# Kernel tuning notes

Measured on AMD Instinct MI355X. Metric: run time of the kernel, lower is better.

The kernel has to match this reference:

```python
import jax, jax.numpy as jnp
import numpy as np

B, N, D, C, Q = 8, 2048, 512, 4096, 4


def l2norm(x):
    return x / jnp.maximum(jnp.linalg.norm(x, axis=-1, keepdims=True), 1e-12)


def rotate_to(src, tgt):
    # rotation-trick transform: rotate src onto tgt, rotation detached
    sg = jax.lax.stop_gradient
    ns = jnp.linalg.norm(src, axis=-1, keepdims=True)
    nt = jnp.linalg.norm(tgt, axis=-1, keepdims=True)
    u = src / ns
    q = tgt / nt
    w = sg(l2norm(u + q))  # Householder bisector, detached
    e = src
    r = (e
         - 2.0 * jnp.sum(e * w, axis=-1, keepdims=True) * w
         + 2.0 * jnp.sum(e * sg(u), axis=-1, keepdims=True) * q)
    return r * sg(nt / ns)


def setup_inputs() -> dict:
    key = jax.random.key(0)
    k1, k2, k3 = jax.random.split(key, 3)
    x = jax.random.normal(k1, (B, N, D), jnp.float32)
    codebooks = jax.random.normal(k2, (Q, C, D), jnp.float32) * D ** -0.5
    weights = jax.random.normal(k3, (Q, D, D), jnp.float32) * D ** -0.5
    return {"x": x, "codebooks": codebooks, "weights": weights}


def reference(x, codebooks, weights):
    sg = jax.lax.stop_gradient
    num_q = codebooks.shape[0]
    residual = x
    quantized_out = jnp.zeros_like(x)
    all_idx, all_loss = [], []
    for i in range(num_q):
        implicit_cb = codebooks[i] @ weights[i].T  # Linear(dim,dim,bias=False)
        cb_n = l2norm(implicit_cb)                 # [C, D]
        x_n = l2norm(residual)                     # [B, N, D]
        # argmax of cosine similarity (no_grad in torch)
        sim = jnp.einsum('bnd,cd->bnc', sg(x_n), sg(cb_n))
        idx = jnp.argmax(sim, axis=-1)             # [B, N]
        quant = cb_n[idx]                          # [B, N, D]
        commit = (jnp.mean((sg(x_n) - quant) ** 2)
                  + 0.25 * jnp.mean((x_n - sg(quant)) ** 2))
        quant = rotate_to(x_n, quant)
        residual = residual - sg(quant)
        quantized_out = quantized_out + quant
        all_idx.append(idx)
        all_loss.append(commit)
    return quantized_out, jnp.stack(all_idx, axis=-1), jnp.stack(all_loss, axis=-1)
```

## Files before the change

kernel.cpp:

```cpp
#include <hip/hip_runtime.h>
#include <math.h>

#define RR 16384
#define DD 512
#define CC 4096
#define QQ 4
#define NB 32
#define NG 64
#define QOUT_SZ (RR*DD)
#define IDX_OFF QOUT_SZ
#define LOSS_OFF (QOUT_SZ + RR*QQ)
#define LOSS_COEF (1.25f / 8388608.0f)
#define NBLK_FIN (RR/4)

#define WS_RESID 0
#define WS_CBN   (RR*DD)
#define WS_RNRM  (WS_CBN + CC*DD)
#define WS_PV    (WS_RNRM + RR)
#define WS_PI    (WS_PV + RR*32*4)
#define WS_F16   (WS_PI + RR*32*4 + 4)
#define F16_A 0
#define F16_B (RR*DD)

typedef _Float16 f16x8 __attribute__((ext_vector_type(8)));
typedef float f32x4 __attribute__((ext_vector_type(4)));

__device__ __forceinline__ float waveSum(float v) {
#pragma unroll
    for (int m = 1; m < 64; m <<= 1) v += __shfl_xor(v, m, 64);
    return v;
}

template <int N>
__device__ __forceinline__ void waveSumN(float* v) {
#pragma unroll
    for (int m = 1; m < 64; m <<= 1) {
#pragma unroll
        for (int j = 0; j < N; ++j) v[j] += __shfl_xor(v[j], m, 64);
    }
}

__device__ __forceinline__ unsigned packKey(float v, int c) {
    unsigned u = __float_as_uint(v);
    u ^= (unsigned)((int)u >> 31) | 0x80000000u;
    return (u & 0xFFFFF000u) | (unsigned)(4095 - c);
}

__device__ __forceinline__ void ceDesc(unsigned &a, unsigned &b) {
    unsigned mn = a > b ? b : a;
    a = a > b ? a : b;
    b = mn;
}

__device__ __forceinline__ void merge4(unsigned k[4],
                                       unsigned b0, unsigned b1,
                                       unsigned b2, unsigned b3) {
    k[0] = k[0] > b3 ? k[0] : b3;
    k[1] = k[1] > b2 ? k[1] : b2;
    k[2] = k[2] > b1 ? k[2] : b1;
    k[3] = k[3] > b0 ? k[3] : b0;
    ceDesc(k[0], k[2]); ceDesc(k[1], k[3]);
    ceDesc(k[0], k[1]); ceDesc(k[2], k[3]);
}

__device__ __forceinline__ void merge4Shfl(unsigned k[4], int m) {
    unsigned b0 = __shfl_xor(k[0], m, 64);
    unsigned b1 = __shfl_xor(k[1], m, 64);
    unsigned b2 = __shfl_xor(k[2], m, 64);
    unsigned b3 = __shfl_xor(k[3], m, 64);
    merge4(k, b0, b1, b2, b3);
}

__global__ void initK(const float* __restrict__ x, float* __restrict__ resid,
                      float* __restrict__ dout) {
    int i = blockIdx.x * blockDim.x + threadIdx.x;
    int stride = gridDim.x * blockDim.x;
    for (; i < QOUT_SZ; i += stride) { resid[i] = x[i]; dout[i] = 0.0f; }
}

__global__ __launch_bounds__(256) void gemmCbK(const float* __restrict__ A,
                                               const float* __restrict__ W,
                                               float* __restrict__ out) {
    __shared__ float As[32][64];
    __shared__ float Bs[32][64];
    int t = threadIdx.x;
    int tx = t & 15, ty = t >> 4;
    int cBase = blockIdx.x * 64;
    int dBase = blockIdx.y * 64;
    int f = t & 7;
    int mq = t >> 3;
    float acc[4][4] = {};
    for (int k0 = 0; k0 < DD; k0 += 32) {
        __syncthreads();
#pragma unroll
        for (int p = 0; p < 2; ++p) {
            int m = mq + p * 32;
            float4 av = *(const float4*)&A[(size_t)(cBase + m) * DD + k0 + f * 4];
            As[f*4+0][m] = av.x; As[f*4+1][m] = av.y; As[f*4+2][m] = av.z; As[f*4+3][m] = av.w;
            float4 wv = *(const float4*)&W[(size_t)(dBase + m) * DD + k0 + f * 4];
            Bs[f*4+0][m] = wv.x; Bs[f*4+1][m] = wv.y; Bs[f*4+2][m] = wv.z; Bs[f*4+3][m] = wv.w;
        }
        __syncthreads();
#pragma unroll
        for (int kk = 0; kk < 32; ++kk) {
            float4 a4 = *(const float4*)&As[kk][ty * 4];
            float4 b4 = *(const float4*)&Bs[kk][tx * 4];
            float a[4] = {a4.x, a4.y, a4.z, a4.w};
            float b[4] = {b4.x, b4.y, b4.z, b4.w};
#pragma unroll
            for (int i = 0; i < 4; ++i)
#pragma unroll
                for (int j = 0; j < 4; ++j) acc[i][j] += a[i] * b[j];
        }
    }
#pragma unroll
    for (int i = 0; i < 4; ++i) {
        float4 v = make_float4(acc[i][0], acc[i][1], acc[i][2], acc[i][3]);
        *(float4*)&out[(size_t)(cBase + ty * 4 + i) * DD + dBase + tx * 4] = v;
    }
}

__global__ void rowNormCvtK(float* __restrict__ buf, _Float16* __restrict__ bf16) {
    int wave = threadIdx.x >> 6, lane = threadIdx.x & 63;
    int row = blockIdx.x * 4 + wave;
    float* p = buf + (size_t)row * DD;
    float4 v0 = *(float4*)&p[lane * 8];
    float4 v1 = *(float4*)&p[lane * 8 + 4];
    float ss = v0.x*v0.x + v0.y*v0.y + v0.z*v0.z + v0.w*v0.w
             + v1.x*v1.x + v1.y*v1.y + v1.z*v1.z + v1.w*v1.w;
    ss = waveSum(ss);
    float nrm = fmaxf(sqrtf(ss), 1e-12f);
    float vals[8] = {v0.x/nrm, v0.y/nrm, v0.z/nrm, v0.w/nrm,
                     v1.x/nrm, v1.y/nrm, v1.z/nrm, v1.w/nrm};
    *(float4*)&p[lane * 8]     = make_float4(vals[0], vals[1], vals[2], vals[3]);
    *(float4*)&p[lane * 8 + 4] = make_float4(vals[4], vals[5], vals[6], vals[7]);
    f16x8 hv;
#pragma unroll
    for (int j = 0; j < 8; ++j) hv[j] = (_Float16)vals[j];
    *(f16x8*)&bf16[(size_t)row * DD + lane * 8] = hv;
}

__global__ void residCvtK(const float* __restrict__ resid,
                          float* __restrict__ rnrm, _Float16* __restrict__ af16) {
    int wave = threadIdx.x >> 6, lane = threadIdx.x & 63;
    int row = blockIdx.x * 4 + wave;
    const float* p = resid + (size_t)row * DD;
    float4 v0 = *(const float4*)&p[lane * 8];
    float4 v1 = *(const float4*)&p[lane * 8 + 4];
    float vals[8] = {v0.x, v0.y, v0.z, v0.w, v1.x, v1.y, v1.z, v1.w};
    float ss = 0.f;
#pragma unroll
    for (int j = 0; j < 8; ++j) ss += vals[j] * vals[j];
    ss = waveSum(ss);
    if (lane == 0) rnrm[row] = fmaxf(sqrtf(ss), 1e-12f);
    f16x8 hv;
#pragma unroll
    for (int j = 0; j < 8; ++j) hv[j] = (_Float16)vals[j];
    *(f16x8*)&af16[(size_t)row * DD + lane * 8] = hv;
}

__global__ __launch_bounds__(512)
void simMfmaK(
    const _Float16* __restrict__ Af16, const _Float16* __restrict__ Bf16,
    unsigned* __restrict__ pk) {
    __shared__ _Float16 Alds[128 * 64];
    __shared__ _Float16 Blds[128 * 64];
    int t = threadIdx.x, w = t >> 6, lane = t & 63;
    int rowBase = blockIdx.x * 128;
    int cBase = blockIdx.y * 128;
    int mbase = (w & 3) * 32, nbase = (w >> 2) * 64;
    int l15 = lane & 15, quad = lane >> 4;

    f32x4 acc[2][4];
#pragma unroll
    for (int i = 0; i < 2; ++i)
#pragma unroll
        for (int j = 0; j < 4; ++j) acc[i][j] = (f32x4){0.f, 0.f, 0.f, 0.f};

    int rsub = lane >> 3;
    int swz = (lane & 7) ^ rsub;

    for (int k0 = 0; k0 < DD; k0 += 64) {
        __syncthreads();
#pragma unroll
        for (int j = 0; j < 2; ++j) {
            int rA = rowBase + j * 64 + 8 * w + rsub;
            int rB = cBase + j * 64 + 8 * w + rsub;
            __builtin_amdgcn_global_load_lds(
                (const __attribute__((address_space(1))) void*)&Af16[(size_t)rA * DD + k0 + swz * 8],
                (__attribute__((address_space(3))) void*)&Alds[(j * 64 + 8 * w) * 64], 16, 0, 0);
            __builtin_amdgcn_global_load_lds(
                (const __attribute__((address_space(1))) void*)&Bf16[(size_t)rB * DD + k0 + swz * 8],
                (__attribute__((address_space(3))) void*)&Blds[(j * 64 + 8 * w) * 64], 16, 0, 0);
        }
        __syncthreads();
#pragma unroll
        for (int kh = 0; kh < 2; ++kh) {
            int chunk = (kh * 4 + quad) ^ (l15 & 7);
            f16x8 af[2];
#pragma unroll
            for (int tm = 0; tm < 2; ++tm)
                af[tm] = *(const f16x8*)&Alds[(mbase + tm * 16 + l15) * 64 + chunk * 8];
#pragma unroll
            for (int tn = 0; tn < 4; ++tn) {
                f16x8 bf = *(const f16x8*)&Blds[(nbase + tn * 16 + l15) * 64 + chunk * 8];
#pragma unroll
                for (int tm = 0; tm < 2; ++tm)
                    acc[tm][tn] = __builtin_amdgcn_mfma_f32_16x16x32_f16(
                        af[tm], bf, acc[tm][tn], 0, 0, 0);
            }
        }
    }

    int gkey = (cBase >> 6) + (w >> 2);
#pragma unroll
    for (int tm = 0; tm < 2; ++tm) {
#pragma unroll
        for (int r = 0; r < 4; ++r) {
            unsigned t0 = packKey(acc[tm][0][r], cBase + nbase + 0 * 16 + l15);
            unsigned t1 = packKey(acc[tm][1][r], cBase + nbase + 1 * 16 + l15);
            unsigned t2 = packKey(acc[tm][2][r], cBase + nbase + 2 * 16 + l15);
            unsigned t3 = packKey(acc[tm][3][r], cBase + nbase + 3 * 16 + l15);
            ceDesc(t0, t1); ceDesc(t2, t3);
            unsigned k0 = t0 > t2 ? t0 : t2;
            unsigned mn = t0 > t2 ? t2 : t0;
            unsigned mx = t1 > t3 ? t1 : t3;
            unsigned k1 = mn > mx ? mn : mx;
#pragma unroll
            for (int m = 1; m < 16; m <<= 1) {
                unsigned b0 = __shfl_xor(k0, m, 64);
                unsigned b1 = __shfl_xor(k1, m, 64);
                unsigned m0 = k0 > b0 ? k0 : b0;
                unsigned n0 = k0 > b0 ? b0 : k0;
                unsigned m1 = k1 > b1 ? k1 : b1;
                k0 = m0;
                k1 = n0 > m1 ? n0 : m1;
            }
            if (l15 == 0) {
                int rowg = rowBase + mbase + tm * 16 + quad * 4 + r;
                *(uint2*)&pk[(size_t)rowg * 128 + gkey * 2] = make_uint2(k0, k1);
            }
        }
    }
}

__global__ void finalizeK(float* __restrict__ resid,
                          float* __restrict__ rnrm,
                          const float* __restrict__ cbn,
                          const unsigned* __restrict__ pk,
                          float* __restrict__ dout,
                          float* __restrict__ lossPart,
                          _Float16* __restrict__ af16, int q) {
    __shared__ float sL[4];
    int wave = threadIdx.x >> 6, lane = threadIdx.x & 63;
    int row = blockIdx.x * 4 + wave;
    float* xr = resid + (size_t)row * DD;
    float nrm = rnrm[row];
    float4 a0 = *(float4*)&xr[lane * 8];
    float4 a1 = *(float4*)&xr[lane * 8 + 4];
    float orig[8] = {a0.x,a0.y,a0.z,a0.w,a1.x,a1.y,a1.z,a1.w};
    float x[8];
#pragma unroll
    for (int j = 0; j < 8; ++j) x[j] = orig[j] / nrm;

    uint2 kp = *(const uint2*)&pk[(size_t)row * 128 + lane * 2];
    unsigned k[4] = {kp.x, kp.y, 0u, 0u};
#pragma unroll
    for (int m = 1; m < 64; m <<= 1) merge4Shfl(k, m);
    int cand[4];
#pragma unroll
    for (int j = 0; j < 4; ++j)
        cand[j] = 4095 - (int)(__shfl(k[j], 0, 64) & 0xFFFu);

    float cv[4][8];
#pragma unroll
    for (int j = 0; j < 4; ++j) {
        const float* cbj = cbn + (size_t)cand[j] * DD;
        float4 c0 = *(const float4*)&cbj[lane * 8];
        float4 c1 = *(const float4*)&cbj[lane * 8 + 4];
        cv[j][0]=c0.x; cv[j][1]=c0.y; cv[j][2]=c0.z; cv[j][3]=c0.w;
        cv[j][4]=c1.x; cv[j][5]=c1.y; cv[j][6]=c1.z; cv[j][7]=c1.w;
    }
    float s[4];
#pragma unroll
    for (int j = 0; j < 4; ++j) {
        float acc = 0.f;
#pragma unroll
        for (int e = 0; e < 8; ++e) acc += x[e] * cv[j][e];
        s[j] = acc;
    }
    waveSumN<4>(s);
    float sBest = -3e38f; int idx = 0x7fffffff, sel = 0;
#pragma unroll
    for (int j = 0; j < 4; ++j) {
        if (s[j] > sBest || (s[j] == sBest && cand[j] < idx)) {
            sBest = s[j]; idx = cand[j]; sel = j;
        }
    }

    float qv[8];
#pragma unroll
    for (int e = 0; e < 8; ++e)
        qv[e] = sel == 0 ? cv[0][e] : sel == 1 ? cv[1][e]
              : sel == 2 ? cv[2][e] : cv[3][e];

    float red3[3] = {0.f, 0.f, 0.f};
#pragma unroll
    for (int j = 0; j < 8; ++j) {
        red3[0] += x[j] * x[j];
        red3[1] += qv[j] * qv[j];
        float d = x[j] - qv[j];
        red3[2] += d * d;
    }
    waveSumN<3>(red3);
    float ns = sqrtf(red3[0]), nt = sqrtf(red3[1]), lrow = red3[2];

    float u[8], qn[8], wv[8];
    float nw2 = 0.f;
#pragma unroll
    for (int j = 0; j < 8; ++j) {
        u[j] = x[j] / ns;
        qn[j] = qv[j] / nt;
        wv[j] = u[j] + qn[j];
        nw2 += wv[j] * wv[j];
    }
    nw2 = waveSum(nw2);
    float nw = fmaxf(sqrtf(nw2), 1e-12f);
    float red2[2] = {0.f, 0.f};
#pragma unroll
    for (int j = 0; j < 8; ++j) {
        wv[j] = wv[j] / nw;
        red2[0] += x[j] * wv[j];
        red2[1] += x[j] * u[j];
    }
    waveSumN<2>(red2);
    float dew = red2[0], deu = red2[1];
    float scale = nt / ns;

    float r[8], nres[8];
    float ss = 0.f;
#pragma unroll
    for (int j = 0; j < 8; ++j) {
        r[j] = (x[j] - 2.0f * dew * wv[j] + 2.0f * deu * qn[j]) * scale;
        nres[j] = orig[j] - r[j];
        ss += nres[j] * nres[j];
    }

    *(float4*)&xr[lane * 8]     = make_float4(nres[0], nres[1], nres[2], nres[3]);
    *(float4*)&xr[lane * 8 + 4] = make_float4(nres[4], nres[5], nres[6], nres[7]);
    ss = waveSum(ss);
    if (lane == 0) rnrm[row] = fmaxf(sqrtf(ss), 1e-12f);
    f16x8 hv;
#pragma unroll
    for (int j = 0; j < 8; ++j) hv[j] = (_Float16)nres[j];
    *(f16x8*)&af16[(size_t)row * DD + lane * 8] = hv;

    float* op = dout + (size_t)row * DD;
    float4 o0 = *(float4*)&op[lane * 8];
    float4 o1 = *(float4*)&op[lane * 8 + 4];
    o0.x += r[0]; o0.y += r[1]; o0.z += r[2]; o0.w += r[3];
    o1.x += r[4]; o1.y += r[5]; o1.z += r[6]; o1.w += r[7];
    *(float4*)&op[lane * 8] = o0;
    *(float4*)&op[lane * 8 + 4] = o1;

    if (lane == 0) {
        dout[IDX_OFF + row * 4 + q] = (float)idx;
        sL[wave] = lrow;
    }
    __syncthreads();
    if (threadIdx.x == 0) {
        lossPart[(size_t)q * NBLK_FIN + blockIdx.x] =
            (sL[0] + sL[1] + sL[2] + sL[3]) * LOSS_COEF;
    }
}

__global__ void lossWriteK(const float* __restrict__ lossPart,
                           float* __restrict__ dout) {
    int q = threadIdx.x >> 6, lane = threadIdx.x & 63;
    float s = 0.f;
    for (int i = lane; i < NBLK_FIN; i += 64)
        s += lossPart[(size_t)q * NBLK_FIN + i];
    s = waveSum(s);
    if (lane == 0) dout[LOSS_OFF + q] = s;
}

extern "C" void kernel_launch(void* const* d_in, const int* in_sizes, int n_in,
                              void* d_out, int out_size, void* d_ws, size_t ws_size,
                              hipStream_t stream) {
    const float* x = (const float*)d_in[0];
    const float* codebooks = (const float*)d_in[1];
    const float* weights = (const float*)d_in[2];
    float* dout = (float*)d_out;
    float* w = (float*)d_ws;

    float* resid = w + WS_RESID;
    float* cbn   = w + WS_CBN;
    float* rnrm  = w + WS_RNRM;
    unsigned* pk = (unsigned*)(w + WS_PV);
    float* lossPart = w + WS_PI;
    _Float16* f16base = (_Float16*)(w + WS_F16);
    _Float16* Af16 = f16base + F16_A;
    _Float16* Bf16 = f16base + F16_B;

    initK<<<4096, 256, 0, stream>>>(x, resid, dout);
    residCvtK<<<RR / 4, 256, 0, stream>>>(resid, rnrm, Af16);

    for (int q = 0; q < QQ; ++q) {
        gemmCbK<<<dim3(CC / 64, DD / 64), 256, 0, stream>>>(
            codebooks + (size_t)q * CC * DD, weights + (size_t)q * DD * DD, cbn);
        rowNormCvtK<<<CC / 4, 256, 0, stream>>>(cbn, Bf16);
        simMfmaK<<<dim3(RR / 128, CC / 128), 512, 0, stream>>>(Af16, Bf16, pk);
        finalizeK<<<RR / 4, 256, 0, stream>>>(resid, rnrm, cbn, pk,
                                              dout, lossPart, Af16, q);
    }
    lossWriteK<<<1, 256, 0, stream>>>(lossPart, dout);
}
```

Before: 891.7 us.

## Replace LDS-staged similarity GEMM with direct global-to-register MFMA loads

The similarity kernel no longer stages A and B tiles through shared memory with barriers. Each wave now loads its MFMA fragments straight from global memory into registers, double-buffered across k-steps. The block tile shrinks to 128x64 with 256 threads, and the launch grid is adjusted to match. This removes LDS traffic and __syncthreads, but it loses the cross-wave reuse that LDS gave: every wave rereads the same B rows from global memory or L2, which raises cache and memory load.

New measurement: 1.844 ms. 2.07x slower.

```diff
diff --git a/kernel.cpp b/kernel.cpp
--- a/kernel.cpp
+++ b/kernel.cpp
@@ -5,7 +5,6 @@
 #define DD 512
 #define CC 4096
 #define QQ 4
-#define NB 32
 #define NG 64
 #define QOUT_SZ (RR*DD)
 #define IDX_OFF QOUT_SZ
@@ -159,16 +158,14 @@
     *(f16x8*)&af16[(size_t)row * DD + lane * 8] = hv;
 }
 
-__global__ __launch_bounds__(512)
+__global__ __launch_bounds__(256)
 void simMfmaK(
     const _Float16* __restrict__ Af16, const _Float16* __restrict__ Bf16,
     unsigned* __restrict__ pk) {
-    __shared__ _Float16 Alds[128 * 64];
-    __shared__ _Float16 Blds[128 * 64];
     int t = threadIdx.x, w = t >> 6, lane = t & 63;
     int rowBase = blockIdx.x * 128;
-    int cBase = blockIdx.y * 128;
-    int mbase = (w & 3) * 32, nbase = (w >> 2) * 64;
+    int cBase = blockIdx.y * 64;
+    int mbase = w * 32;
     int l15 = lane & 15, quad = lane >> 4;
 
     f32x4 acc[2][4];
@@ -177,50 +174,58 @@
 #pragma unroll
         for (int j = 0; j < 4; ++j) acc[i][j] = (f32x4){0.f, 0.f, 0.f, 0.f};
 
-    int rsub = lane >> 3;
-    int swz = (lane & 7) ^ rsub;
-
-    for (int k0 = 0; k0 < DD; k0 += 64) {
-        __syncthreads();
-#pragma unroll
-        for (int j = 0; j < 2; ++j) {
-            int rA = rowBase + j * 64 + 8 * w + rsub;
-            int rB = cBase + j * 64 + 8 * w + rsub;
-            __builtin_amdgcn_global_load_lds(
-                (const __attribute__((address_space(1))) void*)&Af16[(size_t)rA * DD + k0 + swz * 8],
-                (__attribute__((address_space(3))) void*)&Alds[(j * 64 + 8 * w) * 64], 16, 0, 0);
-            __builtin_amdgcn_global_load_lds(
-                (const __attribute__((address_space(1))) void*)&Bf16[(size_t)rB * DD + k0 + swz * 8],
-                (__attribute__((address_space(3))) void*)&Blds[(j * 64 + 8 * w) * 64], 16, 0, 0);
+    const _Float16* A0 = Af16 + (size_t)(rowBase + mbase + l15) * DD + quad * 8;
+    const _Float16* A1 = A0 + 16 * DD;
+    const _Float16* B0 = Bf16 + (size_t)(cBase + l15) * DD + quad * 8;
+    const _Float16* B1 = B0 + 16 * DD;
+    const _Float16* B2 = B0 + 32 * DD;
+    const _Float16* B3 = B0 + 48 * DD;
+
+#define LDSTEP(s) ((s) * 32)
+    f16x8 aA0, aA1, bA0, bA1, bA2, bA3;
+    f16x8 aB0, aB1, bB0, bB1, bB2, bB3;
+
+    aA0 = *(const f16x8*)&A0[LDSTEP(0)]; aA1 = *(const f16x8*)&A1[LDSTEP(0)];
+    bA0 = *(const f16x8*)&B0[LDSTEP(0)]; bA1 = *(const f16x8*)&B1[LDSTEP(0)];
+    bA2 = *(const f16x8*)&B2[LDSTEP(0)]; bA3 = *(const f16x8*)&B3[LDSTEP(0)];
+
+#pragma unroll
+    for (int s = 0; s < 16; s += 2) {
+        aB0 = *(const f16x8*)&A0[LDSTEP(s + 1)]; aB1 = *(const f16x8*)&A1[LDSTEP(s + 1)];
+        bB0 = *(const f16x8*)&B0[LDSTEP(s + 1)]; bB1 = *(const f16x8*)&B1[LDSTEP(s + 1)];
+        bB2 = *(const f16x8*)&B2[LDSTEP(s + 1)]; bB3 = *(const f16x8*)&B3[LDSTEP(s + 1)];
+        acc[0][0] = __builtin_amdgcn_mfma_f32_16x16x32_f16(aA0, bA0, acc[0][0], 0, 0, 0);
+        acc[1][0] = __builtin_amdgcn_mfma_f32_16x16x32_f16(aA1, bA0, acc[1][0], 0, 0, 0);
+        acc[0][1] = __builtin_amdgcn_mfma_f32_16x16x32_f16(aA0, bA1, acc[0][1], 0, 0, 0);
+        acc[1][1] = __builtin_amdgcn_mfma_f32_16x16x32_f16(aA1, bA1, acc[1][1], 0, 0, 0);
+        acc[0][2] = __builtin_amdgcn_mfma_f32_16x16x32_f16(aA0, bA2, acc[0][2], 0, 0, 0);
+        acc[1][2] = __builtin_amdgcn_mfma_f32_16x16x32_f16(aA1, bA2, acc[1][2], 0, 0, 0);
+        acc[0][3] = __builtin_amdgcn_mfma_f32_16x16x32_f16(aA0, bA3, acc[0][3], 0, 0, 0);
+        acc[1][3] = __builtin_amdgcn_mfma_f32_16x16x32_f16(aA1, bA3, acc[1][3], 0, 0, 0);
+        if (s + 2 < 16) {
+            aA0 = *(const f16x8*)&A0[LDSTEP(s + 2)]; aA1 = *(const f16x8*)&A1[LDSTEP(s + 2)];
+            bA0 = *(const f16x8*)&B0[LDSTEP(s + 2)]; bA1 = *(const f16x8*)&B1[LDSTEP(s + 2)];
+            bA2 = *(const f16x8*)&B2[LDSTEP(s + 2)]; bA3 = *(const f16x8*)&B3[LDSTEP(s + 2)];
         }
-        __syncthreads();
-#pragma unroll
-        for (int kh = 0; kh < 2; ++kh) {
-            int chunk = (kh * 4 + quad) ^ (l15 & 7);
-            f16x8 af[2];
-#pragma unroll
-            for (int tm = 0; tm < 2; ++tm)
-                af[tm] = *(const f16x8*)&Alds[(mbase + tm * 16 + l15) * 64 + chunk * 8];
-#pragma unroll
-            for (int tn = 0; tn < 4; ++tn) {
-                f16x8 bf = *(const f16x8*)&Blds[(nbase + tn * 16 + l15) * 64 + chunk * 8];
-#pragma unroll
-                for (int tm = 0; tm < 2; ++tm)
-                    acc[tm][tn] = __builtin_amdgcn_mfma_f32_16x16x32_f16(
-                        af[tm], bf, acc[tm][tn], 0, 0, 0);
-            }
-        }
-    }
-
-    int gkey = (cBase >> 6) + (w >> 2);
+        acc[0][0] = __builtin_amdgcn_mfma_f32_16x16x32_f16(aB0, bB0, acc[0][0], 0, 0, 0);
+        acc[1][0] = __builtin_amdgcn_mfma_f32_16x16x32_f16(aB1, bB0, acc[1][0], 0, 0, 0);
+        acc[0][1] = __builtin_amdgcn_mfma_f32_16x16x32_f16(aB0, bB1, acc[0][1], 0, 0, 0);
+        acc[1][1] = __builtin_amdgcn_mfma_f32_16x16x32_f16(aB1, bB1, acc[1][1], 0, 0, 0);
+        acc[0][2] = __builtin_amdgcn_mfma_f32_16x16x32_f16(aB0, bB2, acc[0][2], 0, 0, 0);
+        acc[1][2] = __builtin_amdgcn_mfma_f32_16x16x32_f16(aB1, bB2, acc[1][2], 0, 0, 0);
+        acc[0][3] = __builtin_amdgcn_mfma_f32_16x16x32_f16(aB0, bB3, acc[0][3], 0, 0, 0);
+        acc[1][3] = __builtin_amdgcn_mfma_f32_16x16x32_f16(aB1, bB3, acc[1][3], 0, 0, 0);
+    }
+
+    int gkey = blockIdx.y;
 #pragma unroll
     for (int tm = 0; tm < 2; ++tm) {
 #pragma unroll
         for (int r = 0; r < 4; ++r) {
-            unsigned t0 = packKey(acc[tm][0][r], cBase + nbase + 0 * 16 + l15);
-            unsigned t1 = packKey(acc[tm][1][r], cBase + nbase + 1 * 16 + l15);
-            unsigned t2 = packKey(acc[tm][2][r], cBase + nbase + 2 * 16 + l15);
-            unsigned t3 = packKey(acc[tm][3][r], cBase + nbase + 3 * 16 + l15);
+            unsigned t0 = packKey(acc[tm][0][r], cBase + 0 * 16 + l15);
+            unsigned t1 = packKey(acc[tm][1][r], cBase + 1 * 16 + l15);
+            unsigned t2 = packKey(acc[tm][2][r], cBase + 2 * 16 + l15);
+            unsigned t3 = packKey(acc[tm][3][r], cBase + 3 * 16 + l15);
             ceDesc(t0, t1); ceDesc(t2, t3);
             unsigned k0 = t0 > t2 ? t0 : t2;
             unsigned mn = t0 > t2 ? t2 : t0;
@@ -409,7 +414,7 @@
         gemmCbK<<<dim3(CC / 64, DD / 64), 256, 0, stream>>>(
             codebooks + (size_t)q * CC * DD, weights + (size_t)q * DD * DD, cbn);
         rowNormCvtK<<<CC / 4, 256, 0, stream>>>(cbn, Bf16);
-        simMfmaK<<<dim3(RR / 128, CC / 128), 512, 0, stream>>>(Af16, Bf16, pk);
+        simMfmaK<<<dim3(RR / 128, CC / 64), 256, 0, stream>>>(Af16, Bf16, pk);
         finalizeK<<<RR / 4, 256, 0, stream>>>(resid, rnrm, cbn, pk,
                                               dout, lossPart, Af16, q);
     }
```

## Use split-bf16 MFMA for codebook projection GEMM and derive output from residual

Applied to the files above, without the earlier changes.

Replaces the fp32 SIMT codebook×weight GEMM with a bf16 MFMA kernel that uses a hi/lo split (three MFMAs per tile) to keep near-fp32 accuracy. Operands are pre-split by a new conversion kernel and loaded into swizzled LDS via global_load_lds. It also drops the per-stage read-modify-write accumulation of the quantized output. Instead the output is computed once at the end as x minus the final residual. This saves three full passes over the output, but adds conversion launches and exposes the result to bf16-split rounding error.

New measurement: 778.4 us. 1.15x faster.

```diff
diff --git a/kernel.cpp b/kernel.cpp
--- a/kernel.cpp
+++ b/kernel.cpp
@@ -5,8 +5,6 @@
 #define DD 512
 #define CC 4096
 #define QQ 4
-#define NB 32
-#define NG 64
 #define QOUT_SZ (RR*DD)
 #define IDX_OFF QOUT_SZ
 #define LOSS_OFF (QOUT_SZ + RR*QQ)
@@ -23,6 +21,7 @@
 #define F16_B (RR*DD)
 
 typedef _Float16 f16x8 __attribute__((ext_vector_type(8)));
+typedef short bf16x8 __attribute__((ext_vector_type(8)));
 typedef float f32x4 __attribute__((ext_vector_type(4)));
 
 __device__ __forceinline__ float waveSum(float v) {
@@ -71,53 +70,114 @@
     merge4(k, b0, b1, b2, b3);
 }
 
-__global__ void initK(const float* __restrict__ x, float* __restrict__ resid,
-                      float* __restrict__ dout) {
+__device__ __forceinline__ unsigned bf16rne(float x) {
+    unsigned u = __float_as_uint(x);
+    return (u + 0x7FFFu + ((u >> 16) & 1u)) >> 16;
+}
+
+__global__ void initK(const float* __restrict__ x, float* __restrict__ resid) {
     int i = blockIdx.x * blockDim.x + threadIdx.x;
     int stride = gridDim.x * blockDim.x;
-    for (; i < QOUT_SZ; i += stride) { resid[i] = x[i]; dout[i] = 0.0f; }
-}
-
-__global__ __launch_bounds__(256) void gemmCbK(const float* __restrict__ A,
-                                               const float* __restrict__ W,
-                                               float* __restrict__ out) {
-    __shared__ float As[32][64];
-    __shared__ float Bs[32][64];
-    int t = threadIdx.x;
-    int tx = t & 15, ty = t >> 4;
-    int cBase = blockIdx.x * 64;
-    int dBase = blockIdx.y * 64;
-    int f = t & 7;
-    int mq = t >> 3;
-    float acc[4][4] = {};
-    for (int k0 = 0; k0 < DD; k0 += 32) {
+    for (; i < QOUT_SZ; i += stride) resid[i] = x[i];
+}
+
+__global__ void cvtSplitK(const float* __restrict__ src, short* __restrict__ hi,
+                          short* __restrict__ lo, int n) {
+    int i = (blockIdx.x * blockDim.x + threadIdx.x) * 4;
+    int stride = gridDim.x * blockDim.x * 4;
+    for (; i < n; i += stride) {
+        float4 v = *(const float4*)&src[i];
+        float vv[4] = {v.x, v.y, v.z, v.w};
+        short hh[4], ll[4];
+#pragma unroll
+        for (int j = 0; j < 4; ++j) {
+            unsigned hb = bf16rne(vv[j]);
+            float hf = __uint_as_float(hb << 16);
+            hh[j] = (short)hb;
+            ll[j] = (short)bf16rne(vv[j] - hf);
+        }
+        *(short4*)&hi[i] = make_short4(hh[0], hh[1], hh[2], hh[3]);
+        *(short4*)&lo[i] = make_short4(ll[0], ll[1], ll[2], ll[3]);
+    }
+}
+
+__global__ __launch_bounds__(256)
+void gemmCbMfmaK(const short* __restrict__ AHi, const short* __restrict__ ALo,
+                 const short* __restrict__ BHi, const short* __restrict__ BLo,
+                 float* __restrict__ out) {
+    __shared__ short AH[64 * 64], AL[64 * 64];
+    __shared__ short BH[64 * 64], BL[64 * 64];
+    int t = threadIdx.x, w = t >> 6, lane = t & 63;
+    int cBase = blockIdx.x * 64, dBase = blockIdx.y * 64;
+    int mbase = (w & 1) * 32, nbase = (w >> 1) * 32;
+    int l15 = lane & 15, quad = lane >> 4;
+
+    f32x4 acc[2][2];
+#pragma unroll
+    for (int i = 0; i < 2; ++i)
+#pragma unroll
+        for (int j = 0; j < 2; ++j) acc[i][j] = (f32x4){0.f, 0.f, 0.f, 0.f};
+
+    int rsub = lane >> 3;
+    int swz = (lane & 7) ^ rsub;
+
+    for (int k0 = 0; k0 < DD; k0 += 64) {
         __syncthreads();
 #pragma unroll
-        for (int p = 0; p < 2; ++p) {
-            int m = mq + p * 32;
-            float4 av = *(const float4*)&A[(size_t)(cBase + m) * DD + k0 + f * 4];
-            As[f*4+0][m] = av.x; As[f*4+1][m] = av.y; As[f*4+2][m] = av.z; As[f*4+3][m] = av.w;
-            float4 wv = *(const float4*)&W[(size_t)(dBase + m) * DD + k0 + f * 4];
-            Bs[f*4+0][m] = wv.x; Bs[f*4+1][m] = wv.y; Bs[f*4+2][m] = wv.z; Bs[f*4+3][m] = wv.w;
+        for (int j = 0; j < 2; ++j) {
+            int r0 = j * 32 + 8 * w;
+            __builtin_amdgcn_global_load_lds(
+                (const __attribute__((address_space(1))) void*)&AHi[(size_t)(cBase + r0 + rsub) * DD + k0 + swz * 8],
+                (__attribute__((address_space(3))) void*)&AH[r0 * 64], 16, 0, 0);
+            __builtin_amdgcn_global_load_lds(
+                (const __attribute__((address_space(1))) void*)&ALo[(size_t)(cBase + r0 + rsub) * DD + k0 + swz * 8],
+                (__attribute__((address_space(3))) void*)&AL[r0 * 64], 16, 0, 0);
+            __builtin_amdgcn_global_load_lds(
+                (const __attribute__((address_space(1))) void*)&BHi[(size_t)(dBase + r0 + rsub) * DD + k0 + swz * 8],
+                (__attribute__((address_space(3))) void*)&BH[r0 * 64], 16, 0, 0);
+            __builtin_amdgcn_global_load_lds(
+                (const __attribute__((address_space(1))) void*)&BLo[(size_t)(dBase + r0 + rsub) * DD + k0 + swz * 8],
+                (__attribute__((address_space(3))) void*)&BL[r0 * 64], 16, 0, 0);
         }
         __syncthreads();
 #pragma unroll
-        for (int kk = 0; kk < 32; ++kk) {
-            float4 a4 = *(const float4*)&As[kk][ty * 4];
-            float4 b4 = *(const float4*)&Bs[kk][tx * 4];
-            float a[4] = {a4.x, a4.y, a4.z, a4.w};
-            float b[4] = {b4.x, b4.y, b4.z, b4.w};
-#pragma unroll
-            for (int i = 0; i < 4; ++i)
-#pragma unroll
-                for (int j = 0; j < 4; ++j) acc[i][j] += a[i] * b[j];
-        }
-    }
-#pragma unroll
-    for (int i = 0; i < 4; ++i) {
-        float4 v = make_float4(acc[i][0], acc[i][1], acc[i][2], acc[i][3]);
-        *(float4*)&out[(size_t)(cBase + ty * 4 + i) * DD + dBase + tx * 4] = v;
-    }
+        for (int kh = 0; kh < 2; ++kh) {
+            int chunk = (kh * 4 + quad) ^ (l15 & 7);
+            bf16x8 ah[2], al[2], bh[2], bl[2];
+#pragma unroll
+            for (int tm = 0; tm < 2; ++tm) {
+                ah[tm] = *(const bf16x8*)&AH[(mbase + tm * 16 + l15) * 64 + chunk * 8];
+                al[tm] = *(const bf16x8*)&AL[(mbase + tm * 16 + l15) * 64 + chunk * 8];
+            }
+#pragma unroll
+            for (int tn = 0; tn < 2; ++tn) {
+                bh[tn] = *(const bf16x8*)&BH[(nbase + tn * 16 + l15) * 64 + chunk * 8];
+                bl[tn] = *(const bf16x8*)&BL[(nbase + tn * 16 + l15) * 64 + chunk * 8];
+            }
+#pragma unroll
+            for (int tn = 0; tn < 2; ++tn)
+#pragma unroll
+                for (int tm = 0; tm < 2; ++tm) {
+                    acc[tm][tn] = __builtin_amdgcn_mfma_f32_16x16x32_bf16(
+                        ah[tm], bh[tn], acc[tm][tn], 0, 0, 0);
+                    acc[tm][tn] = __builtin_amdgcn_mfma_f32_16x16x32_bf16(
+                        ah[tm], bl[tn], acc[tm][tn], 0, 0, 0);
+                    acc[tm][tn] = __builtin_amdgcn_mfma_f32_16x16x32_bf16(
+                        al[tm], bh[tn], acc[tm][tn], 0, 0, 0);
+                }
+        }
+    }
+
+#pragma unroll
+    for (int tm = 0; tm < 2; ++tm)
+#pragma unroll
+        for (int tn = 0; tn < 2; ++tn)
+#pragma unroll
+            for (int r = 0; r < 4; ++r) {
+                int row = cBase + mbase + tm * 16 + quad * 4 + r;
+                int col = dBase + nbase + tn * 16 + l15;
+                out[(size_t)row * DD + col] = acc[tm][tn][r];
+            }
 }
 
 __global__ void rowNormCvtK(float* __restrict__ buf, _Float16* __restrict__ bf16) {
@@ -355,14 +415,6 @@
     for (int j = 0; j < 8; ++j) hv[j] = (_Float16)nres[j];
     *(f16x8*)&af16[(size_t)row * DD + lane * 8] = hv;
 
-    float* op = dout + (size_t)row * DD;
-    float4 o0 = *(float4*)&op[lane * 8];
-    float4 o1 = *(float4*)&op[lane * 8 + 4];
-    o0.x += r[0]; o0.y += r[1]; o0.z += r[2]; o0.w += r[3];
-    o1.x += r[4]; o1.y += r[5]; o1.z += r[6]; o1.w += r[7];
-    *(float4*)&op[lane * 8] = o0;
-    *(float4*)&op[lane * 8 + 4] = o1;
-
     if (lane == 0) {
         dout[IDX_OFF + row * 4 + q] = (float)idx;
         sL[wave] = lrow;
@@ -372,6 +424,13 @@
         lossPart[(size_t)q * NBLK_FIN + blockIdx.x] =
             (sL[0] + sL[1] + sL[2] + sL[3]) * LOSS_COEF;
     }
+}
+
+__global__ void qoutK(const float* __restrict__ x, const float* __restrict__ resid,
+                      float* __restrict__ dout) {
+    int i = blockIdx.x * blockDim.x + threadIdx.x;
+    int stride = gridDim.x * blockDim.x;
+    for (; i < QOUT_SZ; i += stride) dout[i] = x[i] - resid[i];
 }
 
 __global__ void lossWriteK(const float* __restrict__ lossPart,
@@ -401,17 +460,26 @@
     _Float16* f16base = (_Float16*)(w + WS_F16);
     _Float16* Af16 = f16base + F16_A;
     _Float16* Bf16 = f16base + F16_B;
-
-    initK<<<4096, 256, 0, stream>>>(x, resid, dout);
+    short* cbHi = (short*)(w + WS_PV);
+    short* cbLo = cbHi + (size_t)CC * DD;
+    short* wHi  = (short*)(w + WS_PI + 32768);
+    short* wLo  = wHi + (size_t)DD * DD;
+
+    initK<<<2048, 256, 0, stream>>>(x, resid);
     residCvtK<<<RR / 4, 256, 0, stream>>>(resid, rnrm, Af16);
 
     for (int q = 0; q < QQ; ++q) {
-        gemmCbK<<<dim3(CC / 64, DD / 64), 256, 0, stream>>>(
-            codebooks + (size_t)q * CC * DD, weights + (size_t)q * DD * DD, cbn);
+        cvtSplitK<<<512, 256, 0, stream>>>(codebooks + (size_t)q * CC * DD,
+                                           cbHi, cbLo, CC * DD);
+        cvtSplitK<<<128, 256, 0, stream>>>(weights + (size_t)q * DD * DD,
+                                           wHi, wLo, DD * DD);
+        gemmCbMfmaK<<<dim3(CC / 64, DD / 64), 256, 0, stream>>>(
+            cbHi, cbLo, wHi, wLo, cbn);
         rowNormCvtK<<<CC / 4, 256, 0, stream>>>(cbn, Bf16);
         simMfmaK<<<dim3(RR / 128, CC / 128), 512, 0, stream>>>(Af16, Bf16, pk);
         finalizeK<<<RR / 4, 256, 0, stream>>>(resid, rnrm, cbn, pk,
                                               dout, lossPart, Af16, q);
     }
+    qoutK<<<2048, 256, 0, stream>>>(x, resid, dout);
     lossWriteK<<<1, 256, 0, stream>>>(lossPart, dout);
 }
```
